# Optimization experiments

Measured on AMD Instinct MI355X. Metric: run time of the kernel, lower is better.

Reference implementation:

```python
import jax, jax.numpy as jnp
import numpy as np

B, S, D = 1, 2048, 2048
H, G, HD = 32, 8, 64        # n_heads, n_kv_groups, head_dim
GS = H // G                  # group_size
ROPE_BASE = 10000.0


def _rope_tables(seq_len, head_dim):
    inv_freq = 1.0 / (ROPE_BASE ** (jnp.arange(0, head_dim, 2, dtype=jnp.float32) / head_dim))
    angles = jnp.arange(seq_len, dtype=jnp.float32)[:, None] * inv_freq[None, :]  # [S, HD/2]
    angles = jnp.concatenate([angles, angles], axis=-1)                            # [S, HD]
    return jnp.cos(angles), jnp.sin(angles)


def setup_inputs() -> dict:
    key = jax.random.key(0)
    ks = jax.random.split(key, 5)
    x = jax.random.normal(ks[0], (B, S, D), dtype=jnp.float32)
    mask = jnp.triu(jnp.ones((S, S), dtype=bool), k=1)  # True = masked (causal)
    cos_vals, sin_vals = _rope_tables(S, HD)
    scale = 0.02
    Wq = jax.random.normal(ks[1], (H * HD, D), dtype=jnp.float32) * scale
    Wk = jax.random.normal(ks[2], (G * HD, D), dtype=jnp.float32) * scale
    Wv = jax.random.normal(ks[3], (G * HD, D), dtype=jnp.float32) * scale
    Wo = jax.random.normal(ks[4], (D, H * HD), dtype=jnp.float32) * scale
    return {"x": x, "mask": mask, "cos_vals": cos_vals, "sin_vals": sin_vals,
            "Wq": Wq, "Wk": Wk, "Wv": Wv, "Wo": Wo}


def _apply_rope(t, cos, sin):
    # t: [b, heads, S, HD]; cos/sin: [S, HD]
    half = t.shape[-1] // 2
    t1, t2 = t[..., :half], t[..., half:]
    rotated = jnp.concatenate([-t2, t1], axis=-1)
    return t * cos[None, None] + rotated * sin[None, None]


def reference(x, mask, cos_vals, sin_vals, Wq, Wk, Wv, Wo):
    b, s, _ = x.shape
    q = (x @ Wq.T).reshape(b, s, H, HD).transpose(0, 2, 1, 3)   # [b,H,S,HD]
    k = (x @ Wk.T).reshape(b, s, G, HD).transpose(0, 2, 1, 3)   # [b,G,S,HD]
    v = (x @ Wv.T).reshape(b, s, G, HD).transpose(0, 2, 1, 3)   # [b,G,S,HD]
    q = _apply_rope(q, cos_vals, sin_vals)
    k = _apply_rope(k, cos_vals, sin_vals)
    # Group-broadcast instead of repeat_interleave (same math)
    q = q.reshape(b, G, GS, s, HD)
    scores = jnp.einsum('bghqd,bgkd->bghqk', q, k)              # [b,G,GS,S,S]
    scores = jnp.where(mask[None, None, None], -jnp.inf, scores)
    weights = jax.nn.softmax(scores / np.sqrt(HD).astype(np.float32), axis=-1)
    out = jnp.einsum('bghqk,bgkd->bghqd', weights, v)           # [b,G,GS,S,HD]
    out = out.reshape(b, H, s, HD).transpose(0, 2, 1, 3).reshape(b, s, H * HD)
    return out @ Wo.T
```

## Files before the change

kernel.cpp:

```cpp
#include <hip/hip_runtime.h>
#include <cstddef>
#include <cstdint>

#define S 2048
#define Dm 2048
#define NH 32
#define NG 8
#define HD 64

typedef __attribute__((ext_vector_type(8))) short bf16x8;
typedef __attribute__((ext_vector_type(4))) short bf16x4;
typedef __attribute__((ext_vector_type(4))) float f32x4;

__device__ __forceinline__ float fast_exp2(float x) { return __builtin_amdgcn_exp2f(x); }

__device__ __forceinline__ unsigned short f2bf(float f) {
  unsigned int u = __builtin_bit_cast(unsigned int, f);
  u = (u + 0x7fffu + ((u >> 16) & 1u)) >> 16;
  return (unsigned short)u;
}
__device__ __forceinline__ unsigned int pk2bf(float lo, float hi) {
  unsigned int a = __builtin_bit_cast(unsigned int, lo) + 0x8000u;
  unsigned int b = __builtin_bit_cast(unsigned int, hi) + 0x8000u;
  return (a >> 16) | (b & 0xffff0000u);
}
__device__ __forceinline__ void gl_lds16(const unsigned short* g, unsigned short* l) {
  __builtin_amdgcn_global_load_lds(
      (const __attribute__((address_space(1))) unsigned int*)g,
      (__attribute__((address_space(3))) unsigned int*)l, 16, 0, 0);
}

#define QSC 0.1803368801111601f

__global__ __launch_bounds__(256) void cvt_all(const float* __restrict__ x,
                                               const float* __restrict__ Wq,
                                               const float* __restrict__ Wk,
                                               const float* __restrict__ Wv,
                                               const float* __restrict__ Wo,
                                               unsigned short* __restrict__ xb,
                                               unsigned short* __restrict__ Wcat,
                                               unsigned short* __restrict__ Wob) {
  int i = blockIdx.x * 256 + threadIdx.x;
  const float4* src;
  ushort4* dst;
  if (i < 1048576)      { src = (const float4*)x  + i;             dst = (ushort4*)xb + i; }
  else if (i < 2097152) { src = (const float4*)Wq + (i - 1048576); dst = (ushort4*)Wcat + (i - 1048576); }
  else if (i < 2359296) { src = (const float4*)Wk + (i - 2097152); dst = (ushort4*)Wcat + 1048576 + (i - 2097152); }
  else if (i < 2621440) { src = (const float4*)Wv + (i - 2359296); dst = (ushort4*)Wcat + 1310720 + (i - 2359296); }
  else                  { src = (const float4*)Wo + (i - 2621440); dst = (ushort4*)Wob + (i - 2621440); }
  float4 v = *src;
  ushort4 o;
  o.x = f2bf(v.x); o.y = f2bf(v.y); o.z = f2bf(v.z); o.w = f2bf(v.w);
  *dst = o;
}

__global__ __launch_bounds__(256) void gemm_bf16(const unsigned short* __restrict__ A,
                                                 const unsigned short* __restrict__ B,
                                                 float* __restrict__ Cf,
                                                 unsigned short* __restrict__ Cb,
                                                 unsigned short* __restrict__ VtOut,
                                                 const float* __restrict__ cosv,
                                                 const float* __restrict__ sinv,
                                                 int M, int N, int K) {
  __shared__ __align__(16) unsigned short As[64 * 64];
  __shared__ __align__(16) unsigned short Bs[128 * 64];
  const int tid = threadIdx.x;
  const int lane = tid & 63, wave = tid >> 6;
  const int row0 = blockIdx.y * 64, col0 = blockIdx.x * 128;
  const int wr = (wave >> 1) * 32, wc = (wave & 1) * 64;

  f32x4 acc[2][4];
#pragma unroll
  for (int i = 0; i < 2; i++)
#pragma unroll
    for (int j = 0; j < 4; j++) acc[i][j] = (f32x4){0.f, 0.f, 0.f, 0.f};

  const int arow0 = tid >> 3, aslot0 = ((tid & 7) ^ (arow0 & 7)) * 8;
  const int arow1 = (tid + 256) >> 3, aslot1 = (((tid + 256) & 7) ^ (arow1 & 7)) * 8;
  const int fr = lane & 15, q4 = lane >> 4;

  for (int k0 = 0; k0 < K; k0 += 64) {
    gl_lds16(&A[(size_t)(row0 + arow0) * K + k0 + aslot0], &As[tid * 8]);
    gl_lds16(&A[(size_t)(row0 + arow1) * K + k0 + aslot1], &As[(tid + 256) * 8]);
#pragma unroll
    for (int b = 0; b < 4; b++) {
      int p = tid + b * 256;
      int r = p >> 3, sl = ((p & 7) ^ (r & 7)) * 8;
      gl_lds16(&B[(size_t)(col0 + r) * K + k0 + sl], &Bs[p * 8]);
    }
    __syncthreads();
#pragma unroll
    for (int kk = 0; kk < 2; kk++) {
      bf16x8 af[2], bfr[4];
#pragma unroll
      for (int i = 0; i < 2; i++) {
        int R = wr + i * 16 + fr;
        af[i] = *(const bf16x8*)&As[R * 64 + ((q4 + kk * 4) ^ (R & 7)) * 8];
      }
#pragma unroll
      for (int j = 0; j < 4; j++) {
        int R = wc + j * 16 + fr;
        bfr[j] = *(const bf16x8*)&Bs[R * 64 + ((q4 + kk * 4) ^ (R & 7)) * 8];
      }
#pragma unroll
      for (int i = 0; i < 2; i++)
#pragma unroll
        for (int j = 0; j < 4; j++)
          acc[i][j] = __builtin_amdgcn_mfma_f32_16x16x32_bf16(af[i], bfr[j], acc[i][j], 0, 0, 0);
    }
    __syncthreads();
  }

  const int cc = lane & 15, cr = (lane >> 4) * 4;

  if (cosv) {
#pragma unroll
    for (int i = 0; i < 2; i++) {
      int grb = row0 + wr + i * 16 + cr;
#pragma unroll
      for (int j = 0; j < 2; j++) {
        int gc = col0 + wc + j * 16 + cc;
        if (gc < 2560) {
          int d = j * 16 + cc;
          float qs = (gc < 2048) ? QSC : 1.0f;
#pragma unroll
          for (int r = 0; r < 4; r++) {
            float c = cosv[(grb + r) * 64 + d];
            float s = sinv[(grb + r) * 64 + d];
            float t1 = acc[i][j][r], t2 = acc[i][j + 2][r];
            acc[i][j][r]     = (t1 * c - t2 * s) * qs;
            acc[i][j + 2][r] = (t2 * c + t1 * s) * qs;
          }
        }
      }
    }
  }

#pragma unroll
  for (int i = 0; i < 2; i++)
#pragma unroll
    for (int j = 0; j < 4; j++) {
      int gc = col0 + wc + j * 16 + cc;
#pragma unroll
      for (int r = 0; r < 4; r++) {
        int gr = row0 + wr + i * 16 + cr + r;
        if (cosv) {
          if (gc >= 2560) VtOut[(size_t)(gc - 2560) * 2048 + gr] = f2bf(acc[i][j][r]);
          else            Cb[(size_t)gr * N + gc] = f2bf(acc[i][j][r]);
        } else if (Cf)    Cf[(size_t)gr * N + gc] = acc[i][j][r];
        else              Cb[(size_t)gr * N + gc] = f2bf(acc[i][j][r]);
      }
    }
}

__global__ __launch_bounds__(256, 2) void flash_mfma(const unsigned short* __restrict__ QKV,
                                                     const unsigned short* __restrict__ Vt_g,
                                                     unsigned short* __restrict__ Ob) {
  __shared__ __align__(16) unsigned short Ks[2][64 * 64];
  __shared__ __align__(16) unsigned short Vs[2][64 * 64];

  const int tid = threadIdx.x;
  const int lane = tid & 63, wave = tid >> 6;
  const int m15 = lane & 15, q4 = lane >> 4;

  const int L = blockIdx.x;
  const int h = L & 31, g = h >> 2;
  const int u0 = L >> 5, a = u0 >> 3, b = u0 & 7;
  const int u = (a == 0) ? 15 - b : b;
  const int qb = u * 128;
  const int ntiles = 2 * u + 2;

  bf16x8 qf[2][2];
#pragma unroll
  for (int f = 0; f < 2; f++) {
    const size_t qrow = (size_t)(qb + f * 64 + wave * 16 + m15) * 3072 + h * 64;
    qf[f][0] = *(const bf16x8*)&QKV[qrow + q4 * 8];
    qf[f][1] = *(const bf16x8*)&QKV[qrow + 32 + q4 * 8];
  }

  f32x4 accO[2][4];
  float l_lane[2] = {0.f, 0.f};
#pragma unroll
  for (int f = 0; f < 2; f++)
#pragma unroll
    for (int v = 0; v < 4; v++) accO[f][v] = (f32x4){0.f, 0.f, 0.f, 0.f};

  const int p0 = wave * 128 + lane, p1 = p0 + 64;
  const int sr0 = p0 >> 3, so0 = ((p0 & 7) ^ (sr0 & 7)) * 8;
  const int sr1 = p1 >> 3, so1 = ((p1 & 7) ^ (sr1 & 7)) * 8;

#pragma unroll
  for (int t = 0; t < 2; t++) {
    const int k0 = t * 64;
    gl_lds16(&QKV[(size_t)(k0 + sr0) * 3072 + 2048 + g * 64 + so0], &Ks[t][p0 * 8]);
    gl_lds16(&QKV[(size_t)(k0 + sr1) * 3072 + 2048 + g * 64 + so1], &Ks[t][p1 * 8]);
    gl_lds16(&Vt_g[(size_t)(g * 64 + sr0) * 2048 + k0 + so0], &Vs[t][p0 * 8]);
    gl_lds16(&Vt_g[(size_t)(g * 64 + sr1) * 2048 + k0 + so1], &Vs[t][p1 * 8]);
  }

  for (int t = 0; t < ntiles; t++) {
    if (t + 1 < ntiles) asm volatile("s_waitcnt vmcnt(4)" ::: "memory");
    else                asm volatile("s_waitcnt vmcnt(0)" ::: "memory");
    asm volatile("s_barrier" ::: "memory");

    const unsigned short* Kb = Ks[t & 1];
    const unsigned short* Vb = Vs[t & 1];
    const bool act0 = (t < ntiles - 1);

    f32x4 sc[2][4];
#pragma unroll
    for (int kt = 0; kt < 4; kt++) {
      const int krow = kt * 16 + m15;
      bf16x8 kf0 = *(const bf16x8*)&Kb[krow * 64 + (q4 ^ (krow & 7)) * 8];
      bf16x8 kf1 = *(const bf16x8*)&Kb[krow * 64 + ((q4 + 4) ^ (krow & 7)) * 8];
      f32x4 z1 = (f32x4){0.f, 0.f, 0.f, 0.f};
      z1 = __builtin_amdgcn_mfma_f32_16x16x32_bf16(kf0, qf[1][0], z1, 0, 0, 0);
      sc[1][kt] = __builtin_amdgcn_mfma_f32_16x16x32_bf16(kf1, qf[1][1], z1, 0, 0, 0);
      if (act0) {
        f32x4 z0 = (f32x4){0.f, 0.f, 0.f, 0.f};
        z0 = __builtin_amdgcn_mfma_f32_16x16x32_bf16(kf0, qf[0][0], z0, 0, 0, 0);
        sc[0][kt] = __builtin_amdgcn_mfma_f32_16x16x32_bf16(kf1, qf[0][1], z0, 0, 0, 0);
      }
    }

    bf16x8 pA0[2], pA1[2];
#pragma unroll
    for (int f = 0; f < 2; f++) {
      if (f == 0 && !act0) continue;
      if (t == 2 * u + f) {
        const int qo = wave * 16 + m15;
#pragma unroll
        for (int kt = 0; kt < 4; kt++)
#pragma unroll
          for (int r = 0; r < 4; r++)
            if (kt * 16 + q4 * 4 + r > qo) sc[f][kt][r] = -1e30f;
      }
      float rs = 0.f;
#pragma unroll
      for (int kt = 0; kt < 4; kt++)
#pragma unroll
        for (int r = 0; r < 4; r++) {
          float p = fast_exp2(sc[f][kt][r]);
          sc[f][kt][r] = p;
          rs += p;
        }
      l_lane[f] += rs;

      int4 pa0, pa1;
      pa0.x = pk2bf(sc[f][0][0], sc[f][0][1]); pa0.y = pk2bf(sc[f][0][2], sc[f][0][3]);
      pa0.z = pk2bf(sc[f][1][0], sc[f][1][1]); pa0.w = pk2bf(sc[f][1][2], sc[f][1][3]);
      pa1.x = pk2bf(sc[f][2][0], sc[f][2][1]); pa1.y = pk2bf(sc[f][2][2], sc[f][2][3]);
      pa1.z = pk2bf(sc[f][3][0], sc[f][3][1]); pa1.w = pk2bf(sc[f][3][2], sc[f][3][3]);
      pA0[f] = __builtin_bit_cast(bf16x8, pa0);
      pA1[f] = __builtin_bit_cast(bf16x8, pa1);
    }

#pragma unroll
    for (int vt = 0; vt < 4; vt++) {
      const int vrow = vt * 16 + m15;
      const int base = vrow * 64, sw = vrow & 7, half = (q4 & 1) * 4, c1 = q4 >> 1;
      bf16x4 w00 = *(const bf16x4*)&Vb[base + (c1 ^ sw) * 8 + half];
      bf16x4 w01 = *(const bf16x4*)&Vb[base + ((c1 + 2) ^ sw) * 8 + half];
      bf16x4 w10 = *(const bf16x4*)&Vb[base + ((c1 + 4) ^ sw) * 8 + half];
      bf16x4 w11 = *(const bf16x4*)&Vb[base + ((c1 + 6) ^ sw) * 8 + half];
      bf16x8 vB0 = __builtin_shufflevector(w00, w01, 0, 1, 2, 3, 4, 5, 6, 7);
      bf16x8 vB1 = __builtin_shufflevector(w10, w11, 0, 1, 2, 3, 4, 5, 6, 7);
      accO[1][vt] = __builtin_amdgcn_mfma_f32_16x16x32_bf16(pA0[1], vB0, accO[1][vt], 0, 0, 0);
      accO[1][vt] = __builtin_amdgcn_mfma_f32_16x16x32_bf16(pA1[1], vB1, accO[1][vt], 0, 0, 0);
      if (act0) {
        accO[0][vt] = __builtin_amdgcn_mfma_f32_16x16x32_bf16(pA0[0], vB0, accO[0][vt], 0, 0, 0);
        accO[0][vt] = __builtin_amdgcn_mfma_f32_16x16x32_bf16(pA1[0], vB1, accO[0][vt], 0, 0, 0);
      }
    }

    asm volatile("s_barrier" ::: "memory");
    if (t + 2 < ntiles) {
      const int k2 = (t + 2) * 64;
      unsigned short* Kn = (unsigned short*)Ks[t & 1];
      unsigned short* Vn = (unsigned short*)Vs[t & 1];
      gl_lds16(&QKV[(size_t)(k2 + sr0) * 3072 + 2048 + g * 64 + so0], &Kn[p0 * 8]);
      gl_lds16(&QKV[(size_t)(k2 + sr1) * 3072 + 2048 + g * 64 + so1], &Kn[p1 * 8]);
      gl_lds16(&Vt_g[(size_t)(g * 64 + sr0) * 2048 + k2 + so0], &Vn[p0 * 8]);
      gl_lds16(&Vt_g[(size_t)(g * 64 + sr1) * 2048 + k2 + so1], &Vn[p1 * 8]);
    }
  }

#pragma unroll
  for (int f = 0; f < 2; f++) {
    float lsum = l_lane[f];
    lsum += __shfl_xor(lsum, 16);
    lsum += __shfl_xor(lsum, 32);
    float lr[4];
#pragma unroll
    for (int r = 0; r < 4; r++) lr[r] = 1.0f / __shfl(lsum, q4 * 20 + r);
#pragma unroll
    for (int vt = 0; vt < 4; vt++)
#pragma unroll
      for (int r = 0; r < 4; r++) {
        int row = qb + f * 64 + wave * 16 + q4 * 4 + r;
        Ob[(size_t)row * 2048 + h * 64 + vt * 16 + m15] = f2bf(accO[f][vt][r] * lr[r]);
      }
  }
}

extern "C" void kernel_launch(void* const* d_in, const int* in_sizes, int n_in,
                              void* d_out, int out_size, void* d_ws, size_t ws_size,
                              hipStream_t stream) {
  const float* x    = (const float*)d_in[0];
  const float* cosv = (const float*)d_in[2];
  const float* sinv = (const float*)d_in[3];
  const float* Wq   = (const float*)d_in[4];
  const float* Wk   = (const float*)d_in[5];
  const float* Wv   = (const float*)d_in[6];
  const float* Wo   = (const float*)d_in[7];
  float* out = (float*)d_out;

  unsigned short* xb   = (unsigned short*)d_ws;
  unsigned short* Wcat = xb + (size_t)2048 * 2048;
  unsigned short* Wob  = Wcat + (size_t)3072 * 2048;
  unsigned short* QKV  = Wob + (size_t)2048 * 2048;
  unsigned short* Vt_g = QKV + (size_t)3072 * 2048;

  dim3 blk(256);
  cvt_all<<<14336, blk, 0, stream>>>(x, Wq, Wk, Wv, Wo, xb, Wcat, Wob);
  gemm_bf16<<<dim3(24, 32), blk, 0, stream>>>(xb, Wcat, nullptr, QKV, Vt_g, cosv, sinv, 2048, 3072, 2048);
  flash_mfma<<<512, blk, 0, stream>>>(QKV, Vt_g, xb);
  gemm_bf16<<<dim3(16, 32), blk, 0, stream>>>(xb, Wob, out, nullptr, nullptr, nullptr, nullptr, 2048, 2048, 2048);
}
```

Measured before the change: 220.1 us.

## Double-buffer GEMM LDS tiles with async global-to-LDS prefetch two stages ahead

The bf16 GEMM kernel now keeps two LDS buffers for the A and B tiles. Loads for tile k+2 are issued right after the compute on tile k, and each stage waits with explicit vmcnt/lgkmcnt counters instead of a full __syncthreads, so global loads overlap MFMA work. LDS use per block doubles, which can lower occupancy. An lgkmcnt wait is also added before the barrier in the attention kernel's prefetch path.

```diff
diff --git a/kernel.cpp b/kernel.cpp
--- a/kernel.cpp
+++ b/kernel.cpp
@@ -62,8 +62,8 @@
                                                  const float* __restrict__ cosv,
                                                  const float* __restrict__ sinv,
                                                  int M, int N, int K) {
-  __shared__ __align__(16) unsigned short As[64 * 64];
-  __shared__ __align__(16) unsigned short Bs[128 * 64];
+  __shared__ __align__(16) unsigned short As[2][64 * 64];
+  __shared__ __align__(16) unsigned short Bs[2][128 * 64];
   const int tid = threadIdx.x;
   const int lane = tid & 63, wave = tid >> 6;
   const int row0 = blockIdx.y * 64, col0 = blockIdx.x * 128;
@@ -79,28 +79,40 @@
   const int arow1 = (tid + 256) >> 3, aslot1 = (((tid + 256) & 7) ^ (arow1 & 7)) * 8;
   const int fr = lane & 15, q4 = lane >> 4;
 
-  for (int k0 = 0; k0 < K; k0 += 64) {
-    gl_lds16(&A[(size_t)(row0 + arow0) * K + k0 + aslot0], &As[tid * 8]);
-    gl_lds16(&A[(size_t)(row0 + arow1) * K + k0 + aslot1], &As[(tid + 256) * 8]);
+  const int NIT = K >> 6;
+
+#pragma unroll
+  for (int t = 0; t < 2; t++) {
+    const int k0 = t * 64;
+    gl_lds16(&A[(size_t)(row0 + arow0) * K + k0 + aslot0], &As[t][tid * 8]);
+    gl_lds16(&A[(size_t)(row0 + arow1) * K + k0 + aslot1], &As[t][(tid + 256) * 8]);
 #pragma unroll
     for (int b = 0; b < 4; b++) {
       int p = tid + b * 256;
       int r = p >> 3, sl = ((p & 7) ^ (r & 7)) * 8;
-      gl_lds16(&B[(size_t)(col0 + r) * K + k0 + sl], &Bs[p * 8]);
-    }
-    __syncthreads();
+      gl_lds16(&B[(size_t)(col0 + r) * K + k0 + sl], &Bs[t][p * 8]);
+    }
+  }
+
+  for (int it = 0; it < NIT; it++) {
+    if (it + 1 < NIT) asm volatile("s_waitcnt vmcnt(6)" ::: "memory");
+    else              asm volatile("s_waitcnt vmcnt(0)" ::: "memory");
+    asm volatile("s_barrier" ::: "memory");
+
+    const unsigned short* Ab = As[it & 1];
+    const unsigned short* Bb = Bs[it & 1];
 #pragma unroll
     for (int kk = 0; kk < 2; kk++) {
       bf16x8 af[2], bfr[4];
 #pragma unroll
       for (int i = 0; i < 2; i++) {
         int R = wr + i * 16 + fr;
-        af[i] = *(const bf16x8*)&As[R * 64 + ((q4 + kk * 4) ^ (R & 7)) * 8];
+        af[i] = *(const bf16x8*)&Ab[R * 64 + ((q4 + kk * 4) ^ (R & 7)) * 8];
       }
 #pragma unroll
       for (int j = 0; j < 4; j++) {
         int R = wc + j * 16 + fr;
-        bfr[j] = *(const bf16x8*)&Bs[R * 64 + ((q4 + kk * 4) ^ (R & 7)) * 8];
+        bfr[j] = *(const bf16x8*)&Bb[R * 64 + ((q4 + kk * 4) ^ (R & 7)) * 8];
       }
 #pragma unroll
       for (int i = 0; i < 2; i++)
@@ -108,7 +120,22 @@
         for (int j = 0; j < 4; j++)
           acc[i][j] = __builtin_amdgcn_mfma_f32_16x16x32_bf16(af[i], bfr[j], acc[i][j], 0, 0, 0);
     }
-    __syncthreads();
+
+    asm volatile("s_waitcnt lgkmcnt(0)" ::: "memory");
+    asm volatile("s_barrier" ::: "memory");
+    if (it + 2 < NIT) {
+      const int k2 = (it + 2) * 64;
+      unsigned short* An = (unsigned short*)As[it & 1];
+      unsigned short* Bn = (unsigned short*)Bs[it & 1];
+      gl_lds16(&A[(size_t)(row0 + arow0) * K + k2 + aslot0], &An[tid * 8]);
+      gl_lds16(&A[(size_t)(row0 + arow1) * K + k2 + aslot1], &An[(tid + 256) * 8]);
+#pragma unroll
+      for (int b = 0; b < 4; b++) {
+        int p = tid + b * 256;
+        int r = p >> 3, sl = ((p & 7) ^ (r & 7)) * 8;
+        gl_lds16(&B[(size_t)(col0 + r) * K + k2 + sl], &Bn[p * 8]);
+      }
+    }
   }
 
   const int cc = lane & 15, cr = (lane >> 4) * 4;
@@ -273,6 +300,7 @@
       }
     }
 
+    asm volatile("s_waitcnt lgkmcnt(0)" ::: "memory");
     asm volatile("s_barrier" ::: "memory");
     if (t + 2 < ntiles) {
       const int k2 = (t + 2) * 64;
```

New measurement: 220.4 us. No clear change (+0.1%).
